# Optimization experiments

Measured on AMD Instinct MI355X. Metric: run time of the kernel, lower is better.

Reference implementation:

```python
import jax, jax.numpy as jnp
import numpy as np

NODE_SIZE = 500000
LINK_SIZE = 500
DIM = 128
NORM_P = 1
MARGIN = 1.0
BATCH = 16384


def setup_inputs() -> dict:
    key = jax.random.key(0)
    k1, k2, k3, k4, k5, k6, k7, k8 = jax.random.split(key, 8)
    ur_e = 6.0 / np.sqrt(DIM)
    ur_m = 6.0 / DIM
    node_w = jax.random.uniform(k1, (NODE_SIZE, DIM), jnp.float32, -ur_e, ur_e)
    link_w = jax.random.uniform(k2, (LINK_SIZE, DIM), jnp.float32, -ur_e, ur_e)
    transfer_w = jax.random.uniform(k3, (LINK_SIZE, DIM * DIM), jnp.float32, -ur_m, ur_m)
    sp = jax.random.randint(k4, (BATCH,), 0, NODE_SIZE)
    tp = jax.random.randint(k5, (BATCH,), 0, NODE_SIZE)
    sn = jax.random.randint(k6, (BATCH,), 0, NODE_SIZE)
    tn = jax.random.randint(k7, (BATCH,), 0, NODE_SIZE)
    r = jax.random.randint(k8, (BATCH,), 0, LINK_SIZE)
    return {"node_w": node_w, "link_w": link_w, "transfer_w": transfer_w,
            "sp": sp, "tp": tp, "sn": sn, "tn": tn, "r": r}


def _distance(node_w, link_w, transfer_w, s, r, t):
    # gather embeddings
    s_emb = node_w[s]                      # [B, D]
    t_emb = node_w[t]                      # [B, D]
    r_emb = link_w[r]                      # [B, D]
    M = transfer_w[r].reshape(-1, DIM, DIM)  # [B, D, D]
    # per-sample (1xD)x(DxD) matvec: e @ M
    s_proj = jnp.einsum('bd,bde->be', s_emb, M)
    t_proj = jnp.einsum('bd,bde->be', t_emb, M)
    diff = s_proj + r_emb - t_proj
    if NORM_P == 1:
        return jnp.sum(jnp.abs(diff), axis=1)
    return jnp.sum(jnp.abs(diff) ** NORM_P, axis=1) ** (1.0 / NORM_P)


def reference(node_w, link_w, transfer_w, sp, tp, sn, tn, r):
    pos = _distance(node_w, link_w, transfer_w, sp, r, tp)
    neg = _distance(node_w, link_w, transfer_w, sn, r, tn)
    # MarginRankingLoss with target = -1: max(0, (pos - neg) + margin)
    loss = jnp.maximum(pos - neg + MARGIN, 0.0)
    return jnp.mean(loss)
```

## Files before the change

### kernel.cpp

```cpp
#include <hip/hip_runtime.h>

#define BATCH 16384
#define DIM 128
#define NLINK 500
#define NS 16
#define DP_STRIDE 132
#define CAP 128

__device__ __forceinline__ void gload_lds16(const float* g, float* l) {
    __builtin_amdgcn_global_load_lds(
        (const __attribute__((address_space(1))) void*)g,
        (__attribute__((address_space(3))) void*)l, 16, 0, 0);
}

__global__ void k_init(float* __restrict__ out) {
    if (threadIdx.x == 0) out[0] = 0.0f;
}

__global__ __launch_bounds__(512, 2) void k_fused(
    const float* __restrict__ node_w, const float* __restrict__ link_w,
    const float* __restrict__ transfer_w,
    const int* __restrict__ sp, const int* __restrict__ tp,
    const int* __restrict__ sn, const int* __restrict__ tn,
    const int* __restrict__ r, float* __restrict__ out)
{
    __shared__ float Ms[DIM * DIM];
    __shared__ float dp[NS * DP_STRIDE];
    __shared__ float dn[NS * DP_STRIDE];
    __shared__ float remb[DIM];
    __shared__ int   slist[CAP];
    __shared__ int   cnt;
    __shared__ float lossbuf[NS];

    const int link = blockIdx.x;
    const int t = threadIdx.x;
    const int g = t >> 5;
    const int q = t & 31;

    if (t == 0) cnt = 0;
    __syncthreads();

    int4 rv[8];
    #pragma unroll
    for (int j = 0; j < 8; j++) rv[j] = ((const int4*)r)[j * 512 + t];

    {
        const float* src = transfer_w + (size_t)link * (DIM * DIM);
        #pragma unroll
        for (int i = 0; i < 8; i++) {
            const int c = (t + 512 * i) * 4;
            gload_lds16(src + c, Ms + c);
        }
    }
    float4 rl;
    if (t < 32) rl = ((const float4*)(link_w + (size_t)link * DIM))[q];

    #pragma unroll
    for (int j = 0; j < 8; j++) {
        const int bi = (j * 512 + t) * 4;
        if (rv[j].x == link) slist[atomicAdd(&cnt, 1)] = bi;
        if (rv[j].y == link) slist[atomicAdd(&cnt, 1)] = bi + 1;
        if (rv[j].z == link) slist[atomicAdd(&cnt, 1)] = bi + 2;
        if (rv[j].w == link) slist[atomicAdd(&cnt, 1)] = bi + 3;
    }
    if (t < 32) ((float4*)remb)[q] = rl;
    __syncthreads();

    const int count = cnt;
    float* dpr = dp + g * DP_STRIDE;
    float* dnr = dn + g * DP_STRIDE;
    const float4* M4 = (const float4*)Ms;
    float groupSum = 0.0f;

    for (int k = 0; k < count; k += NS) {
        const bool active = (k + g < count);
        if (active) {
            const int b = slist[k + g];
            const float4* A = (const float4*)(node_w + (size_t)sp[b] * DIM);
            const float4* C = (const float4*)(node_w + (size_t)tp[b] * DIM);
            float4 a0 = A[q], c0 = C[q];
            float4 w;
            w.x = a0.x - c0.x; w.y = a0.y - c0.y; w.z = a0.z - c0.z; w.w = a0.w - c0.w;
            ((float4*)dpr)[q] = w;
            const float4* E = (const float4*)(node_w + (size_t)sn[b] * DIM);
            const float4* F = (const float4*)(node_w + (size_t)tn[b] * DIM);
            float4 e0 = E[q], f0 = F[q];
            w.x = e0.x - f0.x; w.y = e0.y - f0.y; w.z = e0.z - f0.z; w.w = e0.w - f0.w;
            ((float4*)dnr)[q] = w;
        }

        float4 accp = {0.f, 0.f, 0.f, 0.f};
        float4 accn = {0.f, 0.f, 0.f, 0.f};
        #pragma unroll 4
        for (int d4 = 0; d4 < 32; d4++) {
            float4 vp = ((const float4*)dpr)[d4];
            float4 vn = ((const float4*)dnr)[d4];
            float4 m0 = M4[(4 * d4 + 0) * 32 + q];
            float4 m1 = M4[(4 * d4 + 1) * 32 + q];
            float4 m2 = M4[(4 * d4 + 2) * 32 + q];
            float4 m3 = M4[(4 * d4 + 3) * 32 + q];
            accp.x = fmaf(m0.x, vp.x, accp.x); accp.y = fmaf(m0.y, vp.x, accp.y);
            accp.z = fmaf(m0.z, vp.x, accp.z); accp.w = fmaf(m0.w, vp.x, accp.w);
            accn.x = fmaf(m0.x, vn.x, accn.x); accn.y = fmaf(m0.y, vn.x, accn.y);
            accn.z = fmaf(m0.z, vn.x, accn.z); accn.w = fmaf(m0.w, vn.x, accn.w);
            accp.x = fmaf(m1.x, vp.y, accp.x); accp.y = fmaf(m1.y, vp.y, accp.y);
            accp.z = fmaf(m1.z, vp.y, accp.z); accp.w = fmaf(m1.w, vp.y, accp.w);
            accn.x = fmaf(m1.x, vn.y, accn.x); accn.y = fmaf(m1.y, vn.y, accn.y);
            accn.z = fmaf(m1.z, vn.y, accn.z); accn.w = fmaf(m1.w, vn.y, accn.w);
            accp.x = fmaf(m2.x, vp.z, accp.x); accp.y = fmaf(m2.y, vp.z, accp.y);
            accp.z = fmaf(m2.z, vp.z, accp.z); accp.w = fmaf(m2.w, vp.z, accp.w);
            accn.x = fmaf(m2.x, vn.z, accn.x); accn.y = fmaf(m2.y, vn.z, accn.y);
            accn.z = fmaf(m2.z, vn.z, accn.z); accn.w = fmaf(m2.w, vn.z, accn.w);
            accp.x = fmaf(m3.x, vp.w, accp.x); accp.y = fmaf(m3.y, vp.w, accp.y);
            accp.z = fmaf(m3.z, vp.w, accp.z); accp.w = fmaf(m3.w, vp.w, accp.w);
            accn.x = fmaf(m3.x, vn.w, accn.x); accn.y = fmaf(m3.y, vn.w, accn.y);
            accn.z = fmaf(m3.z, vn.w, accn.z); accn.w = fmaf(m3.w, vn.w, accn.w);
        }

        float4 re = ((const float4*)remb)[q];
        float v = fabsf(accp.x + re.x) + fabsf(accp.y + re.y)
                + fabsf(accp.z + re.z) + fabsf(accp.w + re.w)
                - fabsf(accn.x + re.x) - fabsf(accn.y + re.y)
                - fabsf(accn.z + re.z) - fabsf(accn.w + re.w);
        #pragma unroll
        for (int o = 16; o >= 1; o >>= 1) v += __shfl_xor(v, o, 32);
        if (active && q == 0) groupSum += fmaxf(v + 1.0f, 0.0f);
    }

    if (q == 0) lossbuf[g] = groupSum;
    __syncthreads();
    if (t == 0) {
        float s = 0.0f;
        #pragma unroll
        for (int i = 0; i < NS; i++) s += lossbuf[i];
        atomicAdd(out, s * (1.0f / BATCH));
    }
}

extern "C" void kernel_launch(void* const* d_in, const int* in_sizes, int n_in,
                              void* d_out, int out_size, void* d_ws, size_t ws_size,
                              hipStream_t stream) {
    const float* node_w     = (const float*)d_in[0];
    const float* link_w     = (const float*)d_in[1];
    const float* transfer_w = (const float*)d_in[2];
    const int* sp = (const int*)d_in[3];
    const int* tp = (const int*)d_in[4];
    const int* sn = (const int*)d_in[5];
    const int* tn = (const int*)d_in[6];
    const int* r  = (const int*)d_in[7];
    float* out = (float*)d_out;
    (void)d_ws; (void)ws_size;

    k_init<<<1, 64, 0, stream>>>(out);
    k_fused<<<NLINK, 512, 0, stream>>>(node_w, link_w, transfer_w,
                                       sp, tp, sn, tn, r, out);
}
```

Before: 341.7 us.

## Process two samples per warp-group and prefetch next gathers during matvec

```diff
diff --git a/kernel.cpp b/kernel.cpp
--- a/kernel.cpp
+++ b/kernel.cpp
@@ -16,6 +16,10 @@
 __global__ void k_init(float* __restrict__ out) {
     if (threadIdx.x == 0) out[0] = 0.0f;
 }
+
+#define FMA4(acc, m, s)                                          \
+    acc.x = fmaf(m.x, s, acc.x); acc.y = fmaf(m.y, s, acc.y);    \
+    acc.z = fmaf(m.z, s, acc.z); acc.w = fmaf(m.w, s, acc.w);
 
 __global__ __launch_bounds__(512, 2) void k_fused(
     const float* __restrict__ node_w, const float* __restrict__ link_w,
@@ -25,8 +29,10 @@
     const int* __restrict__ r, float* __restrict__ out)
 {
     __shared__ float Ms[DIM * DIM];
-    __shared__ float dp[NS * DP_STRIDE];
-    __shared__ float dn[NS * DP_STRIDE];
+    __shared__ float dp0[NS * DP_STRIDE];
+    __shared__ float dn0[NS * DP_STRIDE];
+    __shared__ float dp1[NS * DP_STRIDE];
+    __shared__ float dn1[NS * DP_STRIDE];
     __shared__ float remb[DIM];
     __shared__ int   slist[CAP];
     __shared__ int   cnt;
@@ -67,64 +73,107 @@
     __syncthreads();
 
     const int count = cnt;
-    float* dpr = dp + g * DP_STRIDE;
-    float* dnr = dn + g * DP_STRIDE;
+    float* p0r = dp0 + g * DP_STRIDE;
+    float* n0r = dn0 + g * DP_STRIDE;
+    float* p1r = dp1 + g * DP_STRIDE;
+    float* n1r = dn1 + g * DP_STRIDE;
     const float4* M4 = (const float4*)Ms;
     float groupSum = 0.0f;
 
-    for (int k = 0; k < count; k += NS) {
-        const bool active = (k + g < count);
-        if (active) {
-            const int b = slist[k + g];
-            const float4* A = (const float4*)(node_w + (size_t)sp[b] * DIM);
-            const float4* C = (const float4*)(node_w + (size_t)tp[b] * DIM);
-            float4 a0 = A[q], c0 = C[q];
-            float4 w;
-            w.x = a0.x - c0.x; w.y = a0.y - c0.y; w.z = a0.z - c0.z; w.w = a0.w - c0.w;
-            ((float4*)dpr)[q] = w;
-            const float4* E = (const float4*)(node_w + (size_t)sn[b] * DIM);
-            const float4* F = (const float4*)(node_w + (size_t)tn[b] * DIM);
-            float4 e0 = E[q], f0 = F[q];
-            w.x = e0.x - f0.x; w.y = e0.y - f0.y; w.z = e0.z - f0.z; w.w = e0.w - f0.w;
-            ((float4*)dnr)[q] = w;
-        }
-
-        float4 accp = {0.f, 0.f, 0.f, 0.f};
-        float4 accn = {0.f, 0.f, 0.f, 0.f};
+    int myk = g;
+    if (myk < count) {
+        const int b0 = slist[myk];
+        const int b1 = (myk + 16 < count) ? slist[myk + 16] : b0;
+        float4 a0 = ((const float4*)(node_w + (size_t)sp[b0] * DIM))[q];
+        float4 c0 = ((const float4*)(node_w + (size_t)tp[b0] * DIM))[q];
+        float4 e0 = ((const float4*)(node_w + (size_t)sn[b0] * DIM))[q];
+        float4 f0 = ((const float4*)(node_w + (size_t)tn[b0] * DIM))[q];
+        float4 a1 = ((const float4*)(node_w + (size_t)sp[b1] * DIM))[q];
+        float4 c1 = ((const float4*)(node_w + (size_t)tp[b1] * DIM))[q];
+        float4 e1 = ((const float4*)(node_w + (size_t)sn[b1] * DIM))[q];
+        float4 f1 = ((const float4*)(node_w + (size_t)tn[b1] * DIM))[q];
+        float4 w;
+        w.x = a0.x - c0.x; w.y = a0.y - c0.y; w.z = a0.z - c0.z; w.w = a0.w - c0.w;
+        ((float4*)p0r)[q] = w;
+        w.x = e0.x - f0.x; w.y = e0.y - f0.y; w.z = e0.z - f0.z; w.w = e0.w - f0.w;
+        ((float4*)n0r)[q] = w;
+        w.x = a1.x - c1.x; w.y = a1.y - c1.y; w.z = a1.z - c1.z; w.w = a1.w - c1.w;
+        ((float4*)p1r)[q] = w;
+        w.x = e1.x - f1.x; w.y = e1.y - f1.y; w.z = e1.z - f1.z; w.w = e1.w - f1.w;
+        ((float4*)n1r)[q] = w;
+    }
+
+    while (myk < count) {
+        const bool act1 = (myk + 16) < count;
+        const int nk = myk + 32;
+        const bool hn = nk < count;
+        float4 pa0, pc0, pe0, pf0, pa1, pc1, pe1, pf1;
+        if (hn) {
+            const int nb0 = slist[nk];
+            const int nb1 = (nk + 16 < count) ? slist[nk + 16] : nb0;
+            pa0 = ((const float4*)(node_w + (size_t)sp[nb0] * DIM))[q];
+            pc0 = ((const float4*)(node_w + (size_t)tp[nb0] * DIM))[q];
+            pe0 = ((const float4*)(node_w + (size_t)sn[nb0] * DIM))[q];
+            pf0 = ((const float4*)(node_w + (size_t)tn[nb0] * DIM))[q];
+            pa1 = ((const float4*)(node_w + (size_t)sp[nb1] * DIM))[q];
+            pc1 = ((const float4*)(node_w + (size_t)tp[nb1] * DIM))[q];
+            pe1 = ((const float4*)(node_w + (size_t)sn[nb1] * DIM))[q];
+            pf1 = ((const float4*)(node_w + (size_t)tn[nb1] * DIM))[q];
+        }
+
+        float4 ap0 = {0.f,0.f,0.f,0.f}, an0 = {0.f,0.f,0.f,0.f};
+        float4 ap1 = {0.f,0.f,0.f,0.f}, an1 = {0.f,0.f,0.f,0.f};
         #pragma unroll 4
         for (int d4 = 0; d4 < 32; d4++) {
-            float4 vp = ((const float4*)dpr)[d4];
-            float4 vn = ((const float4*)dnr)[d4];
+            float4 vp0 = ((const float4*)p0r)[d4];
+            float4 vn0 = ((const float4*)n0r)[d4];
+            float4 vp1 = ((const float4*)p1r)[d4];
+            float4 vn1 = ((const float4*)n1r)[d4];
             float4 m0 = M4[(4 * d4 + 0) * 32 + q];
             float4 m1 = M4[(4 * d4 + 1) * 32 + q];
             float4 m2 = M4[(4 * d4 + 2) * 32 + q];
             float4 m3 = M4[(4 * d4 + 3) * 32 + q];
-            accp.x = fmaf(m0.x, vp.x, accp.x); accp.y = fmaf(m0.y, vp.x, accp.y);
-            accp.z = fmaf(m0.z, vp.x, accp.z); accp.w = fmaf(m0.w, vp.x, accp.w);
-            accn.x = fmaf(m0.x, vn.x, accn.x); accn.y = fmaf(m0.y, vn.x, accn.y);
-            accn.z = fmaf(m0.z, vn.x, accn.z); accn.w = fmaf(m0.w, vn.x, accn.w);
-            accp.x = fmaf(m1.x, vp.y, accp.x); accp.y = fmaf(m1.y, vp.y, accp.y);
-            accp.z = fmaf(m1.z, vp.y, accp.z); accp.w = fmaf(m1.w, vp.y, accp.w);
-            accn.x = fmaf(m1.x, vn.y, accn.x); accn.y = fmaf(m1.y, vn.y, accn.y);
-            accn.z = fmaf(m1.z, vn.y, accn.z); accn.w = fmaf(m1.w, vn.y, accn.w);
-            accp.x = fmaf(m2.x, vp.z, accp.x); accp.y = fmaf(m2.y, vp.z, accp.y);
-            accp.z = fmaf(m2.z, vp.z, accp.z); accp.w = fmaf(m2.w, vp.z, accp.w);
-            accn.x = fmaf(m2.x, vn.z, accn.x); accn.y = fmaf(m2.y, vn.z, accn.y);
-            accn.z = fmaf(m2.z, vn.z, accn.z); accn.w = fmaf(m2.w, vn.z, accn.w);
-            accp.x = fmaf(m3.x, vp.w, accp.x); accp.y = fmaf(m3.y, vp.w, accp.y);
-            accp.z = fmaf(m3.z, vp.w, accp.z); accp.w = fmaf(m3.w, vp.w, accp.w);
-            accn.x = fmaf(m3.x, vn.w, accn.x); accn.y = fmaf(m3.y, vn.w, accn.y);
-            accn.z = fmaf(m3.z, vn.w, accn.z); accn.w = fmaf(m3.w, vn.w, accn.w);
+            FMA4(ap0, m0, vp0.x) FMA4(an0, m0, vn0.x)
+            FMA4(ap1, m0, vp1.x) FMA4(an1, m0, vn1.x)
+            FMA4(ap0, m1, vp0.y) FMA4(an0, m1, vn0.y)
+            FMA4(ap1, m1, vp1.y) FMA4(an1, m1, vn1.y)
+            FMA4(ap0, m2, vp0.z) FMA4(an0, m2, vn0.z)
+            FMA4(ap1, m2, vp1.z) FMA4(an1, m2, vn1.z)
+            FMA4(ap0, m3, vp0.w) FMA4(an0, m3, vn0.w)
+            FMA4(ap1, m3, vp1.w) FMA4(an1, m3, vn1.w)
         }
 
         float4 re = ((const float4*)remb)[q];
-        float v = fabsf(accp.x + re.x) + fabsf(accp.y + re.y)
-                + fabsf(accp.z + re.z) + fabsf(accp.w + re.w)
-                - fabsf(accn.x + re.x) - fabsf(accn.y + re.y)
-                - fabsf(accn.z + re.z) - fabsf(accn.w + re.w);
+        float v0 = fabsf(ap0.x + re.x) + fabsf(ap0.y + re.y)
+                 + fabsf(ap0.z + re.z) + fabsf(ap0.w + re.w)
+                 - fabsf(an0.x + re.x) - fabsf(an0.y + re.y)
+                 - fabsf(an0.z + re.z) - fabsf(an0.w + re.w);
+        float v1 = fabsf(ap1.x + re.x) + fabsf(ap1.y + re.y)
+                 + fabsf(ap1.z + re.z) + fabsf(ap1.w + re.w)
+                 - fabsf(an1.x + re.x) - fabsf(an1.y + re.y)
+                 - fabsf(an1.z + re.z) - fabsf(an1.w + re.w);
         #pragma unroll
-        for (int o = 16; o >= 1; o >>= 1) v += __shfl_xor(v, o, 32);
-        if (active && q == 0) groupSum += fmaxf(v + 1.0f, 0.0f);
+        for (int o = 16; o >= 1; o >>= 1) {
+            v0 += __shfl_xor(v0, o, 32);
+            v1 += __shfl_xor(v1, o, 32);
+        }
+        if (q == 0) {
+            groupSum += fmaxf(v0 + 1.0f, 0.0f);
+            if (act1) groupSum += fmaxf(v1 + 1.0f, 0.0f);
+        }
+
+        if (hn) {
+            float4 w;
+            w.x = pa0.x - pc0.x; w.y = pa0.y - pc0.y; w.z = pa0.z - pc0.z; w.w = pa0.w - pc0.w;
+            ((float4*)p0r)[q] = w;
+            w.x = pe0.x - pf0.x; w.y = pe0.y - pf0.y; w.z = pe0.z - pf0.z; w.w = pe0.w - pf0.w;
+            ((float4*)n0r)[q] = w;
+            w.x = pa1.x - pc1.x; w.y = pa1.y - pc1.y; w.z = pa1.z - pc1.z; w.w = pa1.w - pc1.w;
+            ((float4*)p1r)[q] = w;
+            w.x = pe1.x - pf1.x; w.y = pe1.y - pf1.y; w.z = pe1.z - pf1.z; w.w = pe1.w - pf1.w;
+            ((float4*)n1r)[q] = w;
+        }
+        myk = nk;
     }
 
     if (q == 0) lossbuf[g] = groupSum;
```

Measured after the change: 339.0 us. No clear change (-0.8%).

## Process four samples per group to reuse transfer-matrix LDS reads

Applied to the files above, without the earlier changes.

```diff
diff --git a/kernel.cpp b/kernel.cpp
--- a/kernel.cpp
+++ b/kernel.cpp
@@ -3,8 +3,7 @@
 #define BATCH 16384
 #define DIM 128
 #define NLINK 500
-#define NS 16
-#define DP_STRIDE 132
+#define NG 16
 #define CAP 128
 
 __device__ __forceinline__ void gload_lds16(const float* g, float* l) {
@@ -17,6 +16,16 @@
     if (threadIdx.x == 0) out[0] = 0.0f;
 }
 
+#define FMA4(acc, m, s)                                          \
+    acc.x = fmaf(m.x, s, acc.x); acc.y = fmaf(m.y, s, acc.y);    \
+    acc.z = fmaf(m.z, s, acc.z); acc.w = fmaf(m.w, s, acc.w);
+
+#define STEP(M_, C_)                                             \
+    FMA4(a0, M_, v0.C_) FMA4(a1, M_, v1.C_)                      \
+    FMA4(a2, M_, v2.C_) FMA4(a3, M_, v3.C_)                      \
+    FMA4(a4, M_, v4.C_) FMA4(a5, M_, v5.C_)                      \
+    FMA4(a6, M_, v6.C_) FMA4(a7, M_, v7.C_)
+
 __global__ __launch_bounds__(512, 2) void k_fused(
     const float* __restrict__ node_w, const float* __restrict__ link_w,
     const float* __restrict__ transfer_w,
@@ -25,12 +34,10 @@
     const int* __restrict__ r, float* __restrict__ out)
 {
     __shared__ float Ms[DIM * DIM];
-    __shared__ float dp[NS * DP_STRIDE];
-    __shared__ float dn[NS * DP_STRIDE];
-    __shared__ float remb[DIM];
+    __shared__ float dv[NG * 8 * DIM];
     __shared__ int   slist[CAP];
     __shared__ int   cnt;
-    __shared__ float lossbuf[NS];
+    __shared__ float lossbuf[NG];
 
     const int link = blockIdx.x;
     const int t = threadIdx.x;
@@ -52,8 +59,6 @@
             gload_lds16(src + c, Ms + c);
         }
     }
-    float4 rl;
-    if (t < 32) rl = ((const float4*)(link_w + (size_t)link * DIM))[q];
 
     #pragma unroll
     for (int j = 0; j < 8; j++) {
@@ -63,76 +68,94 @@
         if (rv[j].z == link) slist[atomicAdd(&cnt, 1)] = bi + 2;
         if (rv[j].w == link) slist[atomicAdd(&cnt, 1)] = bi + 3;
     }
-    if (t < 32) ((float4*)remb)[q] = rl;
     __syncthreads();
 
     const int count = cnt;
-    float* dpr = dp + g * DP_STRIDE;
-    float* dnr = dn + g * DP_STRIDE;
+    float* gbase = dv + (g * 8) * DIM;
     const float4* M4 = (const float4*)Ms;
-    float groupSum = 0.0f;
+    float lsum = 0.0f;
 
-    for (int k = 0; k < count; k += NS) {
-        const bool active = (k + g < count);
-        if (active) {
-            const int b = slist[k + g];
-            const float4* A = (const float4*)(node_w + (size_t)sp[b] * DIM);
-            const float4* C = (const float4*)(node_w + (size_t)tp[b] * DIM);
-            float4 a0 = A[q], c0 = C[q];
-            float4 w;
-            w.x = a0.x - c0.x; w.y = a0.y - c0.y; w.z = a0.z - c0.z; w.w = a0.w - c0.w;
-            ((float4*)dpr)[q] = w;
-            const float4* E = (const float4*)(node_w + (size_t)sn[b] * DIM);
-            const float4* F = (const float4*)(node_w + (size_t)tn[b] * DIM);
-            float4 e0 = E[q], f0 = F[q];
-            w.x = e0.x - f0.x; w.y = e0.y - f0.y; w.z = e0.z - f0.z; w.w = e0.w - f0.w;
-            ((float4*)dnr)[q] = w;
+    for (int u0 = 4 * g; u0 < count; u0 += 4 * NG) {
+        const float4 re = ((const float4*)(link_w + (size_t)link * DIM))[q];
+
+        const int b0 = slist[u0];
+        const int b1 = slist[(u0 + 1 < count) ? u0 + 1 : count - 1];
+        const int b2 = slist[(u0 + 2 < count) ? u0 + 2 : count - 1];
+        const int b3 = slist[(u0 + 3 < count) ? u0 + 3 : count - 1];
+
+        #define ROW(idx) (((const float4*)(node_w + (size_t)(idx) * DIM))[q])
+        float4 A0 = ROW(sp[b0]), C0 = ROW(tp[b0]), E0 = ROW(sn[b0]), F0 = ROW(tn[b0]);
+        float4 A1 = ROW(sp[b1]), C1 = ROW(tp[b1]), E1 = ROW(sn[b1]), F1 = ROW(tn[b1]);
+        float4 A2 = ROW(sp[b2]), C2 = ROW(tp[b2]), E2 = ROW(sn[b2]), F2 = ROW(tn[b2]);
+        float4 A3 = ROW(sp[b3]), C3 = ROW(tp[b3]), E3 = ROW(sn[b3]), F3 = ROW(tn[b3]);
+        #undef ROW
+
+        {
+            float4 w_;
+            #define DIFF(vec, X, Y)                                              \
+                w_.x = X.x - Y.x; w_.y = X.y - Y.y;                              \
+                w_.z = X.z - Y.z; w_.w = X.w - Y.w;                              \
+                ((float4*)(gbase + (vec) * DIM))[q] = w_;
+            DIFF(0, A0, C0) DIFF(1, E0, F0)
+            DIFF(2, A1, C1) DIFF(3, E1, F1)
+            DIFF(4, A2, C2) DIFF(5, E2, F2)
+            DIFF(6, A3, C3) DIFF(7, E3, F3)
+            #undef DIFF
         }
 
-        float4 accp = {0.f, 0.f, 0.f, 0.f};
-        float4 accn = {0.f, 0.f, 0.f, 0.f};
-        #pragma unroll 4
+        float4 a0 = {0,0,0,0}, a1 = {0,0,0,0}, a2 = {0,0,0,0}, a3 = {0,0,0,0};
+        float4 a4 = {0,0,0,0}, a5 = {0,0,0,0}, a6 = {0,0,0,0}, a7 = {0,0,0,0};
+        const float4* V0 = (const float4*)(gbase + 0 * DIM);
+        const float4* V1 = (const float4*)(gbase + 1 * DIM);
+        const float4* V2 = (const float4*)(gbase + 2 * DIM);
+        const float4* V3 = (const float4*)(gbase + 3 * DIM);
+        const float4* V4 = (const float4*)(gbase + 4 * DIM);
+        const float4* V5 = (const float4*)(gbase + 5 * DIM);
+        const float4* V6 = (const float4*)(gbase + 6 * DIM);
+        const float4* V7 = (const float4*)(gbase + 7 * DIM);
+
+        #pragma unroll 2
         for (int d4 = 0; d4 < 32; d4++) {
-            float4 vp = ((const float4*)dpr)[d4];
-            float4 vn = ((const float4*)dnr)[d4];
+            float4 v0 = V0[d4], v1 = V1[d4], v2 = V2[d4], v3 = V3[d4];
+            float4 v4 = V4[d4], v5 = V5[d4], v6 = V6[d4], v7 = V7[d4];
             float4 m0 = M4[(4 * d4 + 0) * 32 + q];
             float4 m1 = M4[(4 * d4 + 1) * 32 + q];
             float4 m2 = M4[(4 * d4 + 2) * 32 + q];
             float4 m3 = M4[(4 * d4 + 3) * 32 + q];
-            accp.x = fmaf(m0.x, vp.x, accp.x); accp.y = fmaf(m0.y, vp.x, accp.y);
-            accp.z = fmaf(m0.z, vp.x, accp.z); accp.w = fmaf(m0.w, vp.x, accp.w);
-            accn.x = fmaf(m0.x, vn.x, accn.x); accn.y = fmaf(m0.y, vn.x, accn.y);
-            accn.z = fmaf(m0.z, vn.x, accn.z); accn.w = fmaf(m0.w, vn.x, accn.w);
-            accp.x = fmaf(m1.x, vp.y, accp.x); accp.y = fmaf(m1.y, vp.y, accp.y);
-            accp.z = fmaf(m1.z, vp.y, accp.z); accp.w = fmaf(m1.w, vp.y, accp.w);
-            accn.x = fmaf(m1.x, vn.y, accn.x); accn.y = fmaf(m1.y, vn.y, accn.y);
-            accn.z = fmaf(m1.z, vn.y, accn.z); accn.w = fmaf(m1.w, vn.y, accn.w);
-            accp.x = fmaf(m2.x, vp.z, accp.x); accp.y = fmaf(m2.y, vp.z, accp.y);
-            accp.z = fmaf(m2.z, vp.z, accp.z); accp.w = fmaf(m2.w, vp.z, accp.w);
-            accn.x = fmaf(m2.x, vn.z, accn.x); accn.y = fmaf(m2.y, vn.z, accn.y);
-            accn.z = fmaf(m2.z, vn.z, accn.z); accn.w = fmaf(m2.w, vn.z, accn.w);
-            accp.x = fmaf(m3.x, vp.w, accp.x); accp.y = fmaf(m3.y, vp.w, accp.y);
-            accp.z = fmaf(m3.z, vp.w, accp.z); accp.w = fmaf(m3.w, vp.w, accp.w);
-            accn.x = fmaf(m3.x, vn.w, accn.x); accn.y = fmaf(m3.y, vn.w, accn.y);
-            accn.z = fmaf(m3.z, vn.w, accn.z); accn.w = fmaf(m3.w, vn.w, accn.w);
+            STEP(m0, x) STEP(m1, y) STEP(m2, z) STEP(m3, w)
         }
 
-        float4 re = ((const float4*)remb)[q];
-        float v = fabsf(accp.x + re.x) + fabsf(accp.y + re.y)
-                + fabsf(accp.z + re.z) + fabsf(accp.w + re.w)
-                - fabsf(accn.x + re.x) - fabsf(accn.y + re.y)
-                - fabsf(accn.z + re.z) - fabsf(accn.w + re.w);
+        #define LOSS(ACp, ACn)                                                   \
+            (fabsf(ACp.x + re.x) + fabsf(ACp.y + re.y) +                         \
+             fabsf(ACp.z + re.z) + fabsf(ACp.w + re.w)                           \
+           - fabsf(ACn.x + re.x) - fabsf(ACn.y + re.y)                           \
+           - fabsf(ACn.z + re.z) - fabsf(ACn.w + re.w))
+        float s0 = LOSS(a0, a1);
+        float s1 = LOSS(a2, a3);
+        float s2 = LOSS(a4, a5);
+        float s3 = LOSS(a6, a7);
+        #undef LOSS
         #pragma unroll
-        for (int o = 16; o >= 1; o >>= 1) v += __shfl_xor(v, o, 32);
-        if (active && q == 0) groupSum += fmaxf(v + 1.0f, 0.0f);
+        for (int o = 16; o >= 1; o >>= 1) {
+            s0 += __shfl_xor(s0, o, 32);
+            s1 += __shfl_xor(s1, o, 32);
+            s2 += __shfl_xor(s2, o, 32);
+            s3 += __shfl_xor(s3, o, 32);
+        }
+        if (q == 0) {
+            lsum += fmaxf(s0 + 1.0f, 0.0f);
+            if (u0 + 1 < count) lsum += fmaxf(s1 + 1.0f, 0.0f);
+            if (u0 + 2 < count) lsum += fmaxf(s2 + 1.0f, 0.0f);
+            if (u0 + 3 < count) lsum += fmaxf(s3 + 1.0f, 0.0f);
+        }
     }
 
-    if (q == 0) lossbuf[g] = groupSum;
+    if (q == 0) lossbuf[g] = lsum;
     __syncthreads();
     if (t == 0) {
         float s = 0.0f;
         #pragma unroll
-        for (int i = 0; i < NS; i++) s += lossbuf[i];
+        for (int i = 0; i < NG; i++) s += lossbuf[i];
         atomicAdd(out, s * (1.0f / BATCH));
     }
 }
```

Result: no change. 346.6 us (+1.4%).
